# Optimization experiments

Hardware: AMD Instinct MI355X
Metric: run time of the kernel (lower is better)

## Reference

```python
import jax, jax.numpy as jnp
import numpy as np

N_NODES = 100000
N_EDGES = 1600000
F_IN = 512
HIDDEN = 16
N_CLASSES = 7


def gcn_layer(h, src, dst, W, b, n_nodes):
    # GCN: out = D^{-1/2} (A + I) D^{-1/2} (h W) + b
    h = h @ W  # transform first (small dim), then aggregate
    loops = jnp.arange(n_nodes, dtype=src.dtype)
    src2 = jnp.concatenate([src, loops])  # add self-loops
    dst2 = jnp.concatenate([dst, loops])
    deg = jax.ops.segment_sum(jnp.ones_like(dst2, dtype=h.dtype), dst2,
                              num_segments=n_nodes)
    dinv = jnp.where(deg > 0, jax.lax.rsqrt(deg), 0.0)
    norm = dinv[src2] * dinv[dst2]  # [E+N]
    msg = h[src2] * norm[:, None]   # gather + scale
    out = jax.ops.segment_sum(msg, dst2, num_segments=n_nodes)  # scatter-add
    return out + b


def setup_inputs() -> dict:
    key = jax.random.key(0)
    k1, k2, k3, k4 = jax.random.split(key, 4)
    x = jax.random.normal(k1, (N_NODES, F_IN), dtype=jnp.float32)
    edge_index = jax.random.randint(k2, (2, N_EDGES), 0, N_NODES, dtype=jnp.int32)
    W0 = jax.random.normal(k3, (F_IN, HIDDEN), dtype=jnp.float32) * (1.0 / np.sqrt(F_IN))
    b0 = jnp.zeros((HIDDEN,), dtype=jnp.float32)
    W1 = jax.random.normal(k4, (HIDDEN, N_CLASSES), dtype=jnp.float32) * (1.0 / np.sqrt(HIDDEN))
    b1 = jnp.zeros((N_CLASSES,), dtype=jnp.float32)
    return {"x": x, "edge_index": edge_index, "W0": W0, "b0": b0, "W1": W1, "b1": b1}


def reference(x, edge_index, W0, b0, W1, b1):
    # inference path: dropout is identity (training=False)
    src, dst = edge_index[0], edge_index[1]
    h = gcn_layer(x, src, dst, W0, b0, N_NODES)
    h = jax.nn.relu(h)
    h = gcn_layer(h, src, dst, W1, b1, N_NODES)
    return h
```

## Files before the change

### kernel.cpp

```cpp
#include <hip/hip_runtime.h>

constexpr int FIN = 512;
constexpr int HID = 16;
constexpr int NC  = 7;


__global__ void k_hist(const int* __restrict__ dst, int* __restrict__ cnt, int E) {
    int e = blockIdx.x * 256 + threadIdx.x;
    if (e < E) atomicAdd(&cnt[dst[e]], 1);
}

__global__ void k_bsum(const int* __restrict__ cnt, int* __restrict__ bsum, int N) {
    int i = blockIdx.x * 256 + threadIdx.x;
    int v = (i < N) ? cnt[i] : 0;
#pragma unroll
    for (int o = 1; o < 64; o <<= 1) v += __shfl_xor(v, o);
    __shared__ int ws_[4];
    if ((threadIdx.x & 63) == 0) ws_[threadIdx.x >> 6] = v;
    __syncthreads();
    if (threadIdx.x == 0) bsum[blockIdx.x] = ws_[0] + ws_[1] + ws_[2] + ws_[3];
}

__global__ void k_scanb(const int* __restrict__ bsum, int* __restrict__ boff, int nb) {
    __shared__ int s[1024];
    int t = threadIdx.x;
    int mine = (t < nb) ? bsum[t] : 0;
    s[t] = mine;
    __syncthreads();
    for (int o = 1; o < 1024; o <<= 1) {
        int v = (t >= o) ? s[t - o] : 0;
        __syncthreads();
        s[t] += v;
        __syncthreads();
    }
    if (t < nb) boff[t] = s[t] - mine;
}

__global__ void k_rowptr(const int* __restrict__ cnt, const int* __restrict__ boff,
                         int* __restrict__ rowptr, int* __restrict__ cursor,
                         float* __restrict__ dinv, int N, int E) {
    int i = blockIdx.x * 256 + threadIdx.x;
    int v = (i < N) ? cnt[i] : 0;
    int lane = threadIdx.x & 63, w = threadIdx.x >> 6;
    int xs = v;
#pragma unroll
    for (int o = 1; o < 64; o <<= 1) {
        int y = __shfl_up(xs, o);
        if (lane >= o) xs += y;
    }
    __shared__ int wsum[4];
    if (lane == 63) wsum[w] = xs;
    __syncthreads();
    int woff = 0;
    for (int k = 0; k < w; ++k) woff += wsum[k];
    if (i < N) {
        int rp = boff[blockIdx.x] + woff + xs - v;
        rowptr[i] = rp;
        cursor[i] = rp;
        dinv[i] = rsqrtf((float)v + 1.0f);
    }
    if (i == N) rowptr[N] = E;
}


__global__ void __launch_bounds__(64) k_xw0_fill(
    const float* __restrict__ x, const float* __restrict__ W0,
    const float* __restrict__ dinv, float* __restrict__ g0, int N, int nbx,
    const int* __restrict__ src, const int* __restrict__ dst,
    int* __restrict__ cursor, int* __restrict__ esrc, int E) {
    if ((int)blockIdx.x >= nbx) {
        int e = (blockIdx.x - nbx) * 64 + threadIdx.x;
        if (e < E) {
            int p = atomicAdd(&cursor[dst[e]], 1);
            esrc[p] = src[e];
        }
        return;
    }

    int row = blockIdx.x * 64 + threadIdx.x;
    int r = row < N ? row : N - 1;
    const float4* xr = (const float4*)(x + (size_t)r * FIN);

    float acc[HID];
#pragma unroll
    for (int j = 0; j < HID; ++j) acc[j] = 0.f;

    float4 A[16], B[16];
#pragma unroll
    for (int i = 0; i < 16; ++i) A[i] = xr[i];
    __builtin_amdgcn_sched_barrier(0);

#pragma unroll
    for (int b = 0; b < 8; ++b) {
        const float4* cur = (b & 1) ? B : A;
        float4* nxt = (b & 1) ? A : B;
        if (b + 1 < 8) {
#pragma unroll
            for (int i = 0; i < 16; ++i) nxt[i] = xr[(b + 1) * 16 + i];
        }
        __builtin_amdgcn_sched_barrier(0);
        const float* wb = W0 + (size_t)b * 64 * HID;
#pragma unroll
        for (int i = 0; i < 16; ++i) {
            const float* w = wb + i * 4 * HID;
            float4 xv = cur[i];
#pragma unroll
            for (int j = 0; j < HID; ++j) {
                acc[j] = fmaf(xv.x, w[j], acc[j]);
                acc[j] = fmaf(xv.y, w[HID + j], acc[j]);
                acc[j] = fmaf(xv.z, w[2 * HID + j], acc[j]);
                acc[j] = fmaf(xv.w, w[3 * HID + j], acc[j]);
            }
        }
        __builtin_amdgcn_sched_barrier(0);
    }

    if (row < N) {
        float dv = dinv[row];
        float4* gp = (float4*)(g0 + (size_t)row * HID);
#pragma unroll
        for (int q = 0; q < 4; ++q) {
            float4 v;
            v.x = acc[q * 4 + 0] * dv;
            v.y = acc[q * 4 + 1] * dv;
            v.z = acc[q * 4 + 2] * dv;
            v.w = acc[q * 4 + 3] * dv;
            gp[q] = v;
        }
    }
}


__global__ void k_pull0(const int* __restrict__ rowptr, const int* __restrict__ esrc,
                        const float* __restrict__ g0, float* __restrict__ s0, int N) {
    int wid = (blockIdx.x * 256 + threadIdx.x) >> 6;
    if (wid >= N) return;
    int lane = threadIdx.x & 63;
    int grp = lane >> 4, j = lane & 15;
    int e0 = rowptr[wid], e1 = rowptr[wid + 1];
    float acc = 0.f;
    for (int base = e0; base < e1; base += 16) {
        int p = base + (lane & 15);
        int v = (p < e1) ? esrc[p] : 0;
#pragma unroll
        for (int u = 0; u < 4; ++u) {
            int k = grp + 4 * u;
            int idx = __shfl(v, k);
            if (base + k < e1) acc += g0[(size_t)idx * HID + j];
        }
    }
    acc += __shfl_xor(acc, 16);
    acc += __shfl_xor(acc, 32);
    if (grp == 0)
        s0[(size_t)wid * HID + j] = acc + g0[(size_t)wid * HID + j];
}

__global__ void k_h1w1(const float* __restrict__ s0, const float* __restrict__ dinv,
                       const float* __restrict__ b0, const float* __restrict__ W1,
                       float* __restrict__ g1, int N) {
    int i = blockIdx.x * 256 + threadIdx.x;
    if (i >= N) return;
    float dv = dinv[i];
    const float4* sp = (const float4*)(s0 + (size_t)i * HID);
    float4 a = sp[0], b = sp[1], c = sp[2], d = sp[3];
    float h[HID] = {a.x, a.y, a.z, a.w, b.x, b.y, b.z, b.w,
                    c.x, c.y, c.z, c.w, d.x, d.y, d.z, d.w};
#pragma unroll
    for (int j = 0; j < HID; ++j) h[j] = fmaxf(fmaf(h[j], dv, b0[j]), 0.f);
    float o[NC];
#pragma unroll
    for (int c2 = 0; c2 < NC; ++c2) o[c2] = 0.f;
#pragma unroll
    for (int j = 0; j < HID; ++j)
#pragma unroll
        for (int c2 = 0; c2 < NC; ++c2)
            o[c2] = fmaf(h[j], W1[j * NC + c2], o[c2]);
#pragma unroll
    for (int c2 = 0; c2 < NC; ++c2)
        g1[(size_t)i * NC + c2] = o[c2] * dv;
}

__global__ void k_pull1(const int* __restrict__ rowptr, const int* __restrict__ esrc,
                        const float* __restrict__ g1, const float* __restrict__ dinv,
                        const float* __restrict__ b1, float* __restrict__ outp, int N) {
    int wid = (blockIdx.x * 256 + threadIdx.x) >> 6;
    if (wid >= N) return;
    int lane = threadIdx.x & 63;
    int grp = lane >> 3, j = lane & 7;
    int e0 = rowptr[wid], e1 = rowptr[wid + 1];
    float acc = 0.f;
    for (int base = e0; base < e1; base += 16) {
        int p = base + (lane & 15);
        int v = (p < e1) ? esrc[p] : 0;
#pragma unroll
        for (int u = 0; u < 2; ++u) {
            int k = grp + 8 * u;
            int idx = __shfl(v, k);
            if (base + k < e1 && j < NC) acc += g1[(size_t)idx * NC + j];
        }
    }
    acc += __shfl_xor(acc, 8);
    acc += __shfl_xor(acc, 16);
    acc += __shfl_xor(acc, 32);
    if (grp == 0 && j < NC)
        outp[(size_t)wid * NC + j] =
            fmaf(acc + g1[(size_t)wid * NC + j], dinv[wid], b1[j]);
}


extern "C" void kernel_launch(void* const* d_in, const int* in_sizes, int n_in,
                              void* d_out, int out_size, void* d_ws, size_t ws_size,
                              hipStream_t stream) {
    const float* x  = (const float*)d_in[0];
    const int*   ei = (const int*)d_in[1];
    const float* W0 = (const float*)d_in[2];
    const float* b0 = (const float*)d_in[3];
    const float* W1 = (const float*)d_in[4];
    const float* b1 = (const float*)d_in[5];
    float* outp = (float*)d_out;

    int N = in_sizes[0] / FIN;
    int E = in_sizes[1] / 2;
    const int* src = ei;
    const int* dst = ei + E;

    float* fws = (float*)d_ws;
    float* g0   = fws;
    float* s0   = fws + (size_t)16 * N;
    float* g1   = fws + (size_t)32 * N;
    float* dinv = fws + (size_t)39 * N;
    int* iws    = (int*)(fws + (size_t)40 * N);
    int* rowptr = iws;
    int* cursor = iws + (N + 1);
    int* cnt    = iws + (2 * N + 1);
    int* bsum   = iws + (3 * N + 1);
    int* boff   = iws + (3 * N + 1 + 1024);
    int* esrc   = iws + (3 * N + 1 + 2048);

    int nb = (N + 255) / 256;
    int nbx = (N + 63) / 64;
    int nbf = (E + 63) / 64;

    hipMemsetAsync(cnt, 0, (size_t)N * sizeof(int), stream);

    k_hist<<<(E + 255) / 256, 256, 0, stream>>>(dst, cnt, E);
    k_bsum<<<nb, 256, 0, stream>>>(cnt, bsum, N);
    k_scanb<<<1, 1024, 0, stream>>>(bsum, boff, nb);
    k_rowptr<<<(N + 1 + 255) / 256, 256, 0, stream>>>(cnt, boff, rowptr, cursor, dinv, N, E);

    k_xw0_fill<<<nbx + nbf, 64, 0, stream>>>(x, W0, dinv, g0, N, nbx,
                                             src, dst, cursor, esrc, E);

    k_pull0<<<(int)(((size_t)N * 64 + 255) / 256), 256, 0, stream>>>(rowptr, esrc, g0, s0, N);
    k_h1w1<<<nb, 256, 0, stream>>>(s0, dinv, b0, W1, g1, N);
    k_pull1<<<(int)(((size_t)N * 64 + 255) / 256), 256, 0, stream>>>(rowptr, esrc, g1, dinv, b1, outp, N);
}
```

Before: 259.9 us.

## Stage x tiles into LDS via async global_load_lds with split-K across waves

Rewrites the x@W0 kernel to use 256-thread blocks where four waves each handle a quarter of each 32-column K chunk. Tiles of x are copied straight into double-buffered, XOR-swizzled LDS with global_load_lds, which gives coalesced row loads in place of per-thread strided row reads. Partial sums are reduced through LDS at the end. The edge-fill branch is also widened to 256 threads. In exchange it adds block barriers per chunk and a final LDS reduction, and the larger LDS footprint per block may limit occupancy.

```diff
diff --git a/kernel.cpp b/kernel.cpp
--- a/kernel.cpp
+++ b/kernel.cpp
@@ -63,13 +63,24 @@
 }
 
 
-__global__ void __launch_bounds__(64) k_xw0_fill(
+constexpr int RPB  = 64;
+constexpr int KCH  = 32;
+constexpr int NCHK = FIN / KCH;
+
+typedef const __attribute__((address_space(1))) void* gas_ptr;
+typedef __attribute__((address_space(3))) void* las_ptr;
+
+__global__ void __launch_bounds__(256) k_xw0_fill(
     const float* __restrict__ x, const float* __restrict__ W0,
     const float* __restrict__ dinv, float* __restrict__ g0, int N, int nbx,
     const int* __restrict__ src, const int* __restrict__ dst,
     int* __restrict__ cursor, int* __restrict__ esrc, int E) {
+    __shared__ float redbuf[256 * 17];
+    float* buf0 = redbuf;
+    float* buf1 = redbuf + 2048;
+
     if ((int)blockIdx.x >= nbx) {
-        int e = (blockIdx.x - nbx) * 64 + threadIdx.x;
+        int e = (blockIdx.x - nbx) * 256 + threadIdx.x;
         if (e < E) {
             int p = atomicAdd(&cursor[dst[e]], 1);
             esrc[p] = src[e];
@@ -77,33 +88,41 @@
         return;
     }
 
-    int row = blockIdx.x * 64 + threadIdx.x;
-    int r = row < N ? row : N - 1;
-    const float4* xr = (const float4*)(x + (size_t)r * FIN);
+    const int tid = threadIdx.x;
+    const int q = tid >> 6;
+    const int r = tid & 63;
+    const int row0 = blockIdx.x * RPB;
+    const int lane = tid & 63;
+
+    auto STAGE = [&](float* buf, int c) {
+#pragma unroll
+        for (int i = 0; i < 2; ++i) {
+            int off = q * 2048 + i * 1024;
+            int row = (off >> 7) + (lane >> 3);
+            int sL = (lane & 7) ^ (row & 7);
+            int grow = row0 + row;
+            if (grow >= N) grow = N - 1;
+            const float* gp = x + (size_t)grow * FIN + c * KCH + sL * 4;
+            __builtin_amdgcn_global_load_lds((gas_ptr)gp,
+                                             (las_ptr)((char*)buf + off), 16, 0, 0);
+        }
+    };
 
     float acc[HID];
 #pragma unroll
     for (int j = 0; j < HID; ++j) acc[j] = 0.f;
 
-    float4 A[16], B[16];
-#pragma unroll
-    for (int i = 0; i < 16; ++i) A[i] = xr[i];
-    __builtin_amdgcn_sched_barrier(0);
-
-#pragma unroll
-    for (int b = 0; b < 8; ++b) {
-        const float4* cur = (b & 1) ? B : A;
-        float4* nxt = (b & 1) ? A : B;
-        if (b + 1 < 8) {
-#pragma unroll
-            for (int i = 0; i < 16; ++i) nxt[i] = xr[(b + 1) * 16 + i];
-        }
-        __builtin_amdgcn_sched_barrier(0);
-        const float* wb = W0 + (size_t)b * 64 * HID;
-#pragma unroll
-        for (int i = 0; i < 16; ++i) {
-            const float* w = wb + i * 4 * HID;
-            float4 xv = cur[i];
+    STAGE(buf0, 0);
+    for (int c = 0; c < NCHK; ++c) {
+        __syncthreads();
+        if (c + 1 < NCHK) STAGE((c & 1) ? buf0 : buf1, c + 1);
+        const float* bufc = (c & 1) ? buf1 : buf0;
+        const float* wbase = W0 + (size_t)(c * KCH + q * 8) * HID;
+#pragma unroll
+        for (int h = 0; h < 2; ++h) {
+            int sl = (q * 2 + h) ^ (r & 7);
+            float4 xv = *(const float4*)(bufc + r * 32 + sl * 4);
+            const float* w = wbase + h * 4 * HID;
 #pragma unroll
             for (int j = 0; j < HID; ++j) {
                 acc[j] = fmaf(xv.x, w[j], acc[j]);
@@ -112,20 +131,29 @@
                 acc[j] = fmaf(xv.w, w[3 * HID + j], acc[j]);
             }
         }
-        __builtin_amdgcn_sched_barrier(0);
-    }
-
-    if (row < N) {
-        float dv = dinv[row];
-        float4* gp = (float4*)(g0 + (size_t)row * HID);
-#pragma unroll
-        for (int q = 0; q < 4; ++q) {
-            float4 v;
-            v.x = acc[q * 4 + 0] * dv;
-            v.y = acc[q * 4 + 1] * dv;
-            v.z = acc[q * 4 + 2] * dv;
-            v.w = acc[q * 4 + 3] * dv;
-            gp[q] = v;
+    }
+
+    __syncthreads();
+#pragma unroll
+    for (int j = 0; j < HID; ++j) redbuf[tid * 17 + j] = acc[j];
+    __syncthreads();
+    if (tid < RPB) {
+        int row = row0 + tid;
+        if (row < N) {
+            float dv = dinv[row];
+            float4* gp = (float4*)(g0 + (size_t)row * HID);
+#pragma unroll
+            for (int qq = 0; qq < 4; ++qq) {
+                float4 v;
+#pragma unroll
+                for (int u = 0; u < 4; ++u) {
+                    int j = qq * 4 + u;
+                    float s = redbuf[tid * 17 + j] + redbuf[(tid + 64) * 17 + j] +
+                              redbuf[(tid + 128) * 17 + j] + redbuf[(tid + 192) * 17 + j];
+                    (&v.x)[u] = s * dv;
+                }
+                gp[qq] = v;
+            }
         }
     }
 }
@@ -238,8 +266,8 @@
     int* esrc   = iws + (3 * N + 1 + 2048);
 
     int nb = (N + 255) / 256;
-    int nbx = (N + 63) / 64;
-    int nbf = (E + 63) / 64;
+    int nbx = (N + RPB - 1) / RPB;
+    int nbf = (E + 255) / 256;
 
     hipMemsetAsync(cnt, 0, (size_t)N * sizeof(int), stream);
 
@@ -248,8 +276,8 @@
     k_scanb<<<1, 1024, 0, stream>>>(bsum, boff, nb);
     k_rowptr<<<(N + 1 + 255) / 256, 256, 0, stream>>>(cnt, boff, rowptr, cursor, dinv, N, E);
 
-    k_xw0_fill<<<nbx + nbf, 64, 0, stream>>>(x, W0, dinv, g0, N, nbx,
-                                             src, dst, cursor, esrc, E);
+    k_xw0_fill<<<nbx + nbf, 256, 0, stream>>>(x, W0, dinv, g0, N, nbx,
+                                              src, dst, cursor, esrc, E);
 
     k_pull0<<<(int)(((size_t)N * 64 + 255) / 256), 256, 0, stream>>>(rowptr, esrc, g0, s0, N);
     k_h1w1<<<nb, 256, 0, stream>>>(s0, dinv, b0, W1, g1, N);
```

Measured after the change: 313.8 us. 20.7% more time.

## Fuse degree histogram with XW0 matmul and split-K rows across four waves

Applied to the files above, without the earlier changes.

Moves the edge degree histogram into the same launch as the X·W0 transform so the memory-bound matmul and the atomic histogram overlap. The dinv scaling that depended on degrees moves into a later kernel, fused with the CSR fill. The matmul now uses 256-thread blocks that split the 512-wide K dimension across four waves and reduce through shared memory, cutting per-thread register buffers. The cost is an extra read-modify-write pass over g0 for scaling, plus LDS traffic for the reduction.

```diff
diff --git a/kernel.cpp b/kernel.cpp
--- a/kernel.cpp
+++ b/kernel.cpp
@@ -4,11 +4,6 @@
 constexpr int HID = 16;
 constexpr int NC  = 7;
 
-
-__global__ void k_hist(const int* __restrict__ dst, int* __restrict__ cnt, int E) {
-    int e = blockIdx.x * 256 + threadIdx.x;
-    if (e < E) atomicAdd(&cnt[dst[e]], 1);
-}
 
 __global__ void k_bsum(const int* __restrict__ cnt, int* __restrict__ bsum, int N) {
     int i = blockIdx.x * 256 + threadIdx.x;
@@ -63,32 +58,32 @@
 }
 
 
-__global__ void __launch_bounds__(64) k_xw0_fill(
+__global__ void __launch_bounds__(256, 4) k_xw0_hist(
     const float* __restrict__ x, const float* __restrict__ W0,
-    const float* __restrict__ dinv, float* __restrict__ g0, int N, int nbx,
-    const int* __restrict__ src, const int* __restrict__ dst,
-    int* __restrict__ cursor, int* __restrict__ esrc, int E) {
+    float* __restrict__ t0, int N, int nbx,
+    const int* __restrict__ dst, int* __restrict__ cnt, int E) {
+    __shared__ float red[256 * 17];
+
     if ((int)blockIdx.x >= nbx) {
-        int e = (blockIdx.x - nbx) * 64 + threadIdx.x;
-        if (e < E) {
-            int p = atomicAdd(&cursor[dst[e]], 1);
-            esrc[p] = src[e];
-        }
+        int e = (blockIdx.x - nbx) * 256 + threadIdx.x;
+        if (e < E) atomicAdd(&cnt[dst[e]], 1);
         return;
     }
 
-    int row = blockIdx.x * 64 + threadIdx.x;
+    const int tid = threadIdx.x;
+    const int w = tid >> 6;
+    const int lane = tid & 63;
+    int row = blockIdx.x * 64 + lane;
     int r = row < N ? row : N - 1;
-    const float4* xr = (const float4*)(x + (size_t)r * FIN);
+    const float4* xr = (const float4*)(x + (size_t)r * FIN + w * 128);
 
     float acc[HID];
 #pragma unroll
     for (int j = 0; j < HID; ++j) acc[j] = 0.f;
 
-    float4 A[16], B[16];
-#pragma unroll
-    for (int i = 0; i < 16; ++i) A[i] = xr[i];
-    __builtin_amdgcn_sched_barrier(0);
+    float4 A[4], B[4];
+#pragma unroll
+    for (int i = 0; i < 4; ++i) A[i] = xr[i];
 
 #pragma unroll
     for (int b = 0; b < 8; ++b) {
@@ -96,37 +91,63 @@
         float4* nxt = (b & 1) ? A : B;
         if (b + 1 < 8) {
 #pragma unroll
-            for (int i = 0; i < 16; ++i) nxt[i] = xr[(b + 1) * 16 + i];
-        }
-        __builtin_amdgcn_sched_barrier(0);
-        const float* wb = W0 + (size_t)b * 64 * HID;
-#pragma unroll
-        for (int i = 0; i < 16; ++i) {
-            const float* w = wb + i * 4 * HID;
+            for (int i = 0; i < 4; ++i) nxt[i] = xr[(b + 1) * 4 + i];
+        }
+        const float* wk = W0 + (size_t)(w * 128 + b * 16) * HID;
+#pragma unroll
+        for (int i = 0; i < 4; ++i) {
             float4 xv = cur[i];
+            const float* w_ = wk + i * 4 * HID;
 #pragma unroll
             for (int j = 0; j < HID; ++j) {
-                acc[j] = fmaf(xv.x, w[j], acc[j]);
-                acc[j] = fmaf(xv.y, w[HID + j], acc[j]);
-                acc[j] = fmaf(xv.z, w[2 * HID + j], acc[j]);
-                acc[j] = fmaf(xv.w, w[3 * HID + j], acc[j]);
+                acc[j] = fmaf(xv.x, w_[j], acc[j]);
+                acc[j] = fmaf(xv.y, w_[HID + j], acc[j]);
+                acc[j] = fmaf(xv.z, w_[2 * HID + j], acc[j]);
+                acc[j] = fmaf(xv.w, w_[3 * HID + j], acc[j]);
             }
         }
-        __builtin_amdgcn_sched_barrier(0);
-    }
-
-    if (row < N) {
-        float dv = dinv[row];
-        float4* gp = (float4*)(g0 + (size_t)row * HID);
-#pragma unroll
-        for (int q = 0; q < 4; ++q) {
-            float4 v;
-            v.x = acc[q * 4 + 0] * dv;
-            v.y = acc[q * 4 + 1] * dv;
-            v.z = acc[q * 4 + 2] * dv;
-            v.w = acc[q * 4 + 3] * dv;
-            gp[q] = v;
-        }
+    }
+
+#pragma unroll
+    for (int j = 0; j < HID; ++j) red[tid * 17 + j] = acc[j];
+    __syncthreads();
+    if (tid < 64) {
+        if (row < N) {
+            float4* gp = (float4*)(t0 + (size_t)row * HID);
+#pragma unroll
+            for (int q = 0; q < 4; ++q) {
+                float4 v;
+#pragma unroll
+                for (int u = 0; u < 4; ++u) {
+                    int j = q * 4 + u;
+                    (&v.x)[u] = red[tid * 17 + j] + red[(tid + 64) * 17 + j] +
+                                red[(tid + 128) * 17 + j] + red[(tid + 192) * 17 + j];
+                }
+                gp[q] = v;
+            }
+        }
+    }
+}
+
+
+__global__ void k_fill_scale(const int* __restrict__ src, const int* __restrict__ dst,
+                             int* __restrict__ cursor, int* __restrict__ esrc, int E,
+                             int nbf, float4* __restrict__ g4,
+                             const float* __restrict__ dinv, int n4) {
+    if ((int)blockIdx.x < nbf) {
+        int e = blockIdx.x * 256 + threadIdx.x;
+        if (e < E) {
+            int p = atomicAdd(&cursor[dst[e]], 1);
+            esrc[p] = src[e];
+        }
+        return;
+    }
+    int t = (blockIdx.x - nbf) * 256 + threadIdx.x;
+    if (t < n4) {
+        float dv = dinv[t >> 2];
+        float4 v = g4[t];
+        v.x *= dv; v.y *= dv; v.z *= dv; v.w *= dv;
+        g4[t] = v;
     }
 }
 
@@ -237,19 +258,23 @@
     int* boff   = iws + (3 * N + 1 + 1024);
     int* esrc   = iws + (3 * N + 1 + 2048);
 
-    int nb = (N + 255) / 256;
+    int nb  = (N + 255) / 256;
     int nbx = (N + 63) / 64;
-    int nbf = (E + 63) / 64;
+    int nbh = (E + 255) / 256;
+    int nbf = (E + 255) / 256;
+    int n4  = 4 * N;
+    int nbs = (n4 + 255) / 256;
 
     hipMemsetAsync(cnt, 0, (size_t)N * sizeof(int), stream);
 
-    k_hist<<<(E + 255) / 256, 256, 0, stream>>>(dst, cnt, E);
+    k_xw0_hist<<<nbx + nbh, 256, 0, stream>>>(x, W0, g0, N, nbx, dst, cnt, E);
+
     k_bsum<<<nb, 256, 0, stream>>>(cnt, bsum, N);
     k_scanb<<<1, 1024, 0, stream>>>(bsum, boff, nb);
     k_rowptr<<<(N + 1 + 255) / 256, 256, 0, stream>>>(cnt, boff, rowptr, cursor, dinv, N, E);
 
-    k_xw0_fill<<<nbx + nbf, 64, 0, stream>>>(x, W0, dinv, g0, N, nbx,
-                                             src, dst, cursor, esrc, E);
+    k_fill_scale<<<nbf + nbs, 256, 0, stream>>>(src, dst, cursor, esrc, E,
+                                                nbf, (float4*)g0, dinv, n4);
 
     k_pull0<<<(int)(((size_t)N * 64 + 255) / 256), 256, 0, stream>>>(rowptr, esrc, g0, s0, N);
     k_h1w1<<<nb, 256, 0, stream>>>(s0, dinv, b0, W1, g1, N);
```

New measurement: 384.3 us. +47.9%, slower.
